# Kernel tuning notes

Hardware: AMD Instinct MI355X
Metric: run time of the kernel (lower is better)

Reference implementation:

```python
import jax, jax.numpy as jnp
import numpy as np

B, S, E, H = 2, 2048, 2048, 16
D = E // H          # head_dim = 128
RD = 128            # rotary_emb_dim (== head_dim here)
BASE = 10000.0


def setup_inputs() -> dict:
    key = jax.random.key(0)
    k1, k2, k3, k4, k5 = jax.random.split(key, 5)
    scale = 0.02
    return {
        "x": jax.random.normal(k1, (B, S, E), dtype=jnp.float32),
        "wqkv_w": jax.random.normal(k2, (3 * E, E), dtype=jnp.float32) * scale,
        "wqkv_b": jax.random.normal(k3, (3 * E,), dtype=jnp.float32) * scale,
        "out_w": jax.random.normal(k4, (E, E), dtype=jnp.float32) * scale,
        "out_b": jax.random.normal(k5, (E,), dtype=jnp.float32) * scale,
    }


def _rope_cos_sin(seqlen, dtype):
    inv_freq = 1.0 / (BASE ** (jnp.arange(0, RD, 2, dtype=jnp.float32) / RD))
    t = jnp.arange(seqlen, dtype=jnp.float32)
    freqs = jnp.outer(t, inv_freq)          # (S, RD//2)
    return jnp.cos(freqs).astype(dtype), jnp.sin(freqs).astype(dtype)


def _apply_rotary(v, cos, sin):
    # v: (B, S, H, D); rotate first RD dims (here RD == D)
    v_rot, v_pass = v[..., :RD], v[..., RD:]
    v1, v2 = jnp.split(v_rot, 2, axis=-1)    # each (B, S, H, RD//2)
    c = cos[None, :, None, :]
    s = sin[None, :, None, :]
    rot = jnp.concatenate([v1 * c - v2 * s, v1 * s + v2 * c], axis=-1)
    return jnp.concatenate([rot, v_pass], axis=-1)


def reference(x, wqkv_w, wqkv_b, out_w, out_b):
    b, s, e = x.shape
    # column-parallel QKV projection (world size 1)
    qkv = jnp.einsum("bse,fe->bsf", x, wqkv_w) + wqkv_b     # (B, S, 3E)
    qkv = qkv.reshape(b, s, 3, H, D)
    cos, sin = _rope_cos_sin(s, x.dtype)
    q = _apply_rotary(qkv[:, :, 0], cos, sin)               # (B, S, H, D)
    k = _apply_rotary(qkv[:, :, 1], cos, sin)
    v = qkv[:, :, 2]
    # causal self-attention, softmax_scale = 1/sqrt(head_dim)
    scale = 1.0 / jnp.sqrt(jnp.asarray(D, dtype=x.dtype))
    scores = jnp.einsum("bshd,bthd->bhst", q, k) * scale    # (B, H, S, S)
    causal_mask = jnp.tril(jnp.ones((s, s), dtype=bool))
    scores = jnp.where(causal_mask[None, None], scores, jnp.finfo(x.dtype).min)
    probs = jax.nn.softmax(scores, axis=-1)
    ctx = jnp.einsum("bhst,bthd->bshd", probs, v)           # (B, S, H, D)
    # row-parallel output projection
    out = jnp.einsum("bse,fe->bsf", ctx.reshape(b, s, e), out_w) + out_b
    return out
```

## Files before the change

### kernel.cpp

```cpp
#include <hip/hip_runtime.h>
#include <cstdint>
#include <cstddef>

#define Bd 2
#define Sd 2048
#define Ed 2048
#define Hd 16
#define Dd 128
#define N3E 6144
#define ATT_SCALE 0.08838834764831845f

typedef short bf16x8 __attribute__((ext_vector_type(8)));
typedef float f32x4 __attribute__((ext_vector_type(4)));

__device__ __forceinline__ float bf2f(unsigned short u) {
    union { unsigned int u; float f; } c;
    c.u = ((unsigned int)u) << 16;
    return c.f;
}
__device__ __forceinline__ unsigned short f2bf(float f) {
    union { float f; unsigned int u; } c;
    c.f = f;
    unsigned int x = c.u;
    x += 0x7FFFu + ((x >> 16) & 1u);
    return (unsigned short)(x >> 16);
}

__device__ __forceinline__ void gl2lds16(const void* g, void* l) {
    __builtin_amdgcn_global_load_lds(
        (const __attribute__((address_space(1))) void*)g,
        (__attribute__((address_space(3))) void*)l, 16, 0, 0);
}

__global__ void cvt_all(const float* __restrict__ x,
                        const float* __restrict__ w1,
                        const float* __restrict__ w2,
                        unsigned short* __restrict__ ox,
                        unsigned short* __restrict__ o1,
                        unsigned short* __restrict__ o2) {
    int i = (blockIdx.x * 256 + threadIdx.x) * 4;
    const float* s;
    unsigned short* d;
    int off;
    if (i < 8388608) { s = x; d = ox; off = i; }
    else if (i < 20971520) { s = w1; d = o1; off = i - 8388608; }
    else { s = w2; d = o2; off = i - 20971520; }
    const float4 v = *(const float4*)(s + off);
    d[off + 0] = f2bf(v.x);
    d[off + 1] = f2bf(v.y);
    d[off + 2] = f2bf(v.z);
    d[off + 3] = f2bf(v.w);
}

template <int MODE>
__global__ void gemm_bt(const unsigned short* __restrict__ A,
                        const unsigned short* __restrict__ Bm,
                        const float* __restrict__ bias,
                        void* __restrict__ o0, void* __restrict__ o1,
                        void* __restrict__ o2, int Ndim, int K) {
    __shared__ __align__(16) unsigned short U[16640];
    unsigned short* As = U;
    unsigned short* Bs = U + 8192;

    const int tid = threadIdx.x;
    const int lane = tid & 63;
    const int wave = tid >> 6;
    const int quad = lane >> 4;
    const int l16 = lane & 15;
    const int wr = wave >> 1;
    const int wc = wave & 1;

    const int n0 = blockIdx.x * 128;
    const int m0 = blockIdx.y * 128;

    const unsigned short* Ab = A + (size_t)m0 * K;
    const unsigned short* Bb = Bm + (size_t)n0 * K;

    const f32x4 fzero = {0.f, 0.f, 0.f, 0.f};
    f32x4 acc[4][4];
#pragma unroll
    for (int i = 0; i < 4; i++)
#pragma unroll
        for (int j = 0; j < 4; j++) acc[i][j] = fzero;

    for (int k0 = 0; k0 < K; k0 += 64) {
        __syncthreads();
#pragma unroll
        for (int it = 0; it < 4; ++it) {
            int L = it * 256 + tid;
            int row = L >> 3;
            int cs = L & 7;
            int gc = cs ^ (row & 7);
            gl2lds16(Ab + row * K + k0 + gc * 8, (void*)(As + L * 8));
            gl2lds16(Bb + row * K + k0 + gc * 8, (void*)(Bs + L * 8));
        }
        __syncthreads();
#pragma unroll
        for (int kk = 0; kk < 2; ++kk) {
            bf16x8 af[4], bfr[4];
#pragma unroll
            for (int i = 0; i < 4; i++) {
                int row = wr * 64 + i * 16 + l16;
                int cs = kk * 4 + quad;
                af[i] = *(const bf16x8*)(As + row * 64 + (cs ^ (row & 7)) * 8);
            }
#pragma unroll
            for (int j = 0; j < 4; j++) {
                int row = wc * 64 + j * 16 + l16;
                int cs = kk * 4 + quad;
                bfr[j] = *(const bf16x8*)(Bs + row * 64 + (cs ^ (row & 7)) * 8);
            }
#pragma unroll
            for (int i = 0; i < 4; i++)
#pragma unroll
                for (int j = 0; j < 4; j++)
                    acc[i][j] = __builtin_amdgcn_mfma_f32_16x16x32_bf16(
                        af[i], bfr[j], acc[i][j], 0, 0, 0);
        }
    }

    if (MODE == 0) {
#pragma unroll
        for (int j = 0; j < 4; j++) {
            int col = n0 + wc * 64 + j * 16 + l16;
            float bv = bias[col];
#pragma unroll
            for (int i = 0; i < 4; i++) {
                int rbase = m0 + wr * 64 + i * 16 + quad * 4;
#pragma unroll
                for (int r = 0; r < 4; r++)
                    ((float*)o0)[(size_t)(rbase + r) * Ndim + col] =
                        acc[i][j][r] + bv;
            }
        }
    } else {
        __syncthreads();
#pragma unroll
        for (int j = 0; j < 4; j++) {
            int coll = wc * 64 + j * 16 + l16;
            float bv = bias[n0 + coll];
#pragma unroll
            for (int i = 0; i < 4; i++) {
                int rl = wr * 64 + i * 16 + quad * 4;
#pragma unroll
                for (int r = 0; r < 4; r++)
                    U[(rl + r) * 130 + coll] = f2bf(acc[i][j][r] + bv);
            }
        }
        __syncthreads();

        const int ch = n0 >> 7;
        const int c = ch >> 4;
        const int h = ch & 15;
        const int bb = m0 >> 11;
        const int s0 = m0 & 2047;

        if (c < 2) {
            unsigned short* dstq = (unsigned short*)(c == 0 ? o0 : o1);
            const size_t hb = ((size_t)(bb * Hd + h)) * Sd;
#pragma unroll
            for (int it = 0; it < 16; ++it) {
                int lin = it * 256 + tid;
                int row = lin >> 5, p = lin & 31;
                int s = s0 + row;
                unsigned int lo = *(const unsigned int*)(U + row * 130 + 2 * p);
                unsigned int hi =
                    *(const unsigned int*)(U + row * 130 + 64 + 2 * p);
                float v1a = bf2f((unsigned short)lo), v1b = bf2f(lo >> 16);
                float v2a = bf2f((unsigned short)hi), v2b = bf2f(hi >> 16);
                float fa = (float)s * __expf(-(float)(2 * p) *
                                             (9.210340371976184f / 64.0f));
                float fb = (float)s * __expf(-(float)(2 * p + 1) *
                                             (9.210340371976184f / 64.0f));
                float sna, csa, snb, csb;
                __sincosf(fa, &sna, &csa);
                __sincosf(fb, &snb, &csb);
                ushort2 r1, r2;
                r1.x = f2bf(v1a * csa - v2a * sna);
                r1.y = f2bf(v1b * csb - v2b * snb);
                r2.x = f2bf(v1a * sna + v2a * csa);
                r2.y = f2bf(v1b * snb + v2b * csb);
                unsigned short* dst = dstq + (hb + s) * Dd;
                *(ushort2*)(dst + 2 * p) = r1;
                *(ushort2*)(dst + 64 + 2 * p) = r2;
            }
        } else {
            unsigned short* dstv = (unsigned short*)o2;
            const size_t hb = ((size_t)(bb * Hd + h)) * Dd;
#pragma unroll
            for (int it = 0; it < 16; ++it) {
                int lin = it * 256 + tid;
                int d = lin >> 5, sc = lin & 31;
                int s4 = sc * 4;
                ushort4 pk;
                pk.x = U[(s4 + 0) * 130 + d];
                pk.y = U[(s4 + 1) * 130 + d];
                pk.z = U[(s4 + 2) * 130 + d];
                pk.w = U[(s4 + 3) * 130 + d];
                *(ushort4*)(dstv + (hb + d) * Sd + s0 + s4) = pk;
            }
        }
    }
}

__global__ __launch_bounds__(256, 4) void flash_attn(
    const unsigned short* __restrict__ q, const unsigned short* __restrict__ k,
    const unsigned short* __restrict__ vt, unsigned short* __restrict__ ctx) {
    __shared__ __align__(16) unsigned short Ks[64 * 128];
    __shared__ __align__(16) unsigned short Vts[128 * 64];
    __shared__ __align__(16) unsigned short Ps[64 * 64];

    const int tid = threadIdx.x;
    const int lane = tid & 63;
    const int wave = tid >> 6;
    const int quad = lane >> 4;
    const int l16 = lane & 15;
    const int rw0 = wave * 16;
    const int ql = rw0 + l16;
    const int qsw = ql & 7;

    const int yy = blockIdx.y;
    const int kq = yy >> 3, y0 = yy & 7;
    const int qi = (kq == 0) ? 31 - y0 : (kq == 1) ? y0 : (kq == 2) ? 23 - y0 : 8 + y0;
    const int bh = blockIdx.x;
    const int q0 = qi * 64;

    const unsigned short* qb = q + ((size_t)bh * Sd + q0) * Dd;
    const unsigned short* kb = k + (size_t)bh * Sd * Dd;
    const unsigned short* vtb = vt + (size_t)bh * Dd * Sd;

#pragma unroll
    for (int it = 0; it < 4; ++it) {
        int L = it * 256 + tid;
        int row = L >> 4;
        int cs = L & 15;
        int gc = cs ^ (row & 15);
        gl2lds16(qb + row * Dd + gc * 8, (void*)(Ks + L * 8));
    }
    __syncthreads();
    bf16x8 aq[4];
#pragma unroll
    for (int kk = 0; kk < 4; kk++)
        aq[kk] = *(const bf16x8*)(Ks + ql * 128 + ((kk * 4 + quad) ^ (ql & 15)) * 8);
    __syncthreads();

    const f32x4 fzero = {0.f, 0.f, 0.f, 0.f};
    f32x4 o[8];
#pragma unroll
    for (int jd = 0; jd < 8; jd++) o[jd] = fzero;
    float mi = -3.0e38f, li = 0.f;

    for (int t0 = 0; t0 <= q0; t0 += 64) {
#pragma unroll
        for (int it = 0; it < 4; ++it) {
            int L = it * 256 + tid;
            int rk = L >> 4;
            int ck = L & 15;
            int gk = ck ^ (rk & 15);
            gl2lds16(kb + (size_t)(t0 + rk) * Dd + gk * 8, (void*)(Ks + L * 8));
            int rv = L >> 3;
            int cv = L & 7;
            int gv = cv ^ (rv & 7);
            gl2lds16(vtb + (size_t)rv * Sd + t0 + gv * 8, (void*)(Vts + L * 8));
        }
        __syncthreads();

        f32x4 sa[4];
#pragma unroll
        for (int j = 0; j < 4; j++) sa[j] = fzero;
#pragma unroll
        for (int kk = 0; kk < 4; kk++) {
            bf16x8 bk[4];
#pragma unroll
            for (int j = 0; j < 4; j++) {
                int rowt = j * 16 + l16;
                bk[j] = *(const bf16x8*)(Ks + rowt * 128 +
                                         ((kk * 4 + quad) ^ (rowt & 15)) * 8);
            }
#pragma unroll
            for (int j = 0; j < 4; j++)
                sa[j] = __builtin_amdgcn_mfma_f32_16x16x32_bf16(bk[j], aq[kk],
                                                                sa[j], 0, 0, 0);
        }

#pragma unroll
        for (int j = 0; j < 4; j++)
#pragma unroll
            for (int r = 0; r < 4; r++) sa[j][r] *= ATT_SCALE;
        if (t0 == q0) {
            const int qg = rw0 + l16;
#pragma unroll
            for (int j = 0; j < 4; j++)
#pragma unroll
                for (int r = 0; r < 4; r++)
                    if ((j * 16 + quad * 4 + r) > qg) sa[j][r] = -3.0e38f;
        }

        float mx = -3.0e38f;
#pragma unroll
        for (int j = 0; j < 4; j++)
#pragma unroll
            for (int r = 0; r < 4; r++) mx = fmaxf(mx, sa[j][r]);
        mx = fmaxf(mx, __shfl_xor(mx, 16, 64));
        mx = fmaxf(mx, __shfl_xor(mx, 32, 64));
        const float mnew = fmaxf(mi, mx);
        const float alpha = __expf(mi - mnew);
        float rs = 0.f;
#pragma unroll
        for (int j = 0; j < 4; j++)
#pragma unroll
            for (int r = 0; r < 4; r++) {
                float pp = __expf(sa[j][r] - mnew);
                sa[j][r] = pp;
                rs += pp;
            }
        rs += __shfl_xor(rs, 16, 64);
        rs += __shfl_xor(rs, 32, 64);
        li = li * alpha + rs;
        mi = mnew;

#pragma unroll
        for (int j = 0; j < 4; j++) {
            ushort4 pk;
            pk.x = f2bf(sa[j][0]);
            pk.y = f2bf(sa[j][1]);
            pk.z = f2bf(sa[j][2]);
            pk.w = f2bf(sa[j][3]);
            *(ushort4*)(Ps + ql * 64 + ((j * 2 + (quad >> 1)) ^ qsw) * 8 +
                        (quad & 1) * 4) = pk;
        }

        float av[4];
#pragma unroll
        for (int r = 0; r < 4; r++) av[r] = __shfl(alpha, quad * 4 + r, 64);
#pragma unroll
        for (int jd = 0; jd < 8; jd++)
#pragma unroll
            for (int r = 0; r < 4; r++) o[jd][r] *= av[r];

#pragma unroll
        for (int kk = 0; kk < 2; kk++) {
            bf16x8 ap = *(const bf16x8*)(Ps + ql * 64 +
                                         ((kk * 4 + quad) ^ qsw) * 8);
            bf16x8 bv[8];
#pragma unroll
            for (int jd = 0; jd < 8; jd++) {
                int d = jd * 16 + l16;
                bv[jd] = *(const bf16x8*)(Vts + d * 64 +
                                          ((kk * 4 + quad) ^ (d & 7)) * 8);
            }
#pragma unroll
            for (int jd = 0; jd < 8; jd++)
                o[jd] = __builtin_amdgcn_mfma_f32_16x16x32_bf16(ap, bv[jd],
                                                                o[jd], 0, 0, 0);
        }
        __syncthreads();
    }

    const int b = bh >> 4;
    const int h = bh & 15;
    float linv[4];
#pragma unroll
    for (int r = 0; r < 4; r++) linv[r] = 1.0f / __shfl(li, quad * 4 + r, 64);
#pragma unroll
    for (int r = 0; r < 4; r++) {
        const int grow = q0 + rw0 + quad * 4 + r;
        unsigned short* dst = ctx + ((size_t)(b * Sd + grow)) * Ed + h * Dd;
#pragma unroll
        for (int jd = 0; jd < 8; jd++)
            dst[jd * 16 + l16] = f2bf(o[jd][r] * linv[r]);
    }
}

extern "C" void kernel_launch(void* const* d_in, const int* in_sizes, int n_in,
                              void* d_out, int out_size, void* d_ws,
                              size_t ws_size, hipStream_t stream) {
    const float* x = (const float*)d_in[0];
    const float* wqkv_w = (const float*)d_in[1];
    const float* wqkv_b = (const float*)d_in[2];
    const float* out_w = (const float*)d_in[3];
    const float* out_b = (const float*)d_in[4];
    float* out = (float*)d_out;

    char* ws = (char*)d_ws;
    unsigned short* xb    = (unsigned short*)(ws + 0);
    unsigned short* wqkvb = (unsigned short*)(ws + 16777216);
    unsigned short* owb   = (unsigned short*)(ws + 41943040);
    unsigned short* qb    = (unsigned short*)(ws + 50331648);
    unsigned short* kb    = (unsigned short*)(ws + 67108864);
    unsigned short* vtb   = (unsigned short*)(ws + 83886080);
    unsigned short* ctx   = (unsigned short*)(ws + 0);

    cvt_all<<<24576, 256, 0, stream>>>(x, wqkv_w, out_w, xb, wqkvb, owb);
    gemm_bt<1><<<dim3(48, 32), 256, 0, stream>>>(xb, wqkvb, wqkv_b, qb, kb, vtb,
                                                 N3E, Ed);
    flash_attn<<<dim3(32, 32), 256, 0, stream>>>(qb, kb, vtb, ctx);
    gemm_bt<0><<<dim3(16, 32), 256, 0, stream>>>(ctx, owb, out_b, out, nullptr,
                                                 nullptr, Ed, Ed);
}
```

Before: 350.8 us.

## Use 128-row query tiles with 32x32 MFMA in flash attention

The flash attention kernel now processes 128 query rows per block (32 per wave) instead of 64, and switches from 16x16x32 to 32x32x16 bf16 MFMA for both QK^T and PV. Q is loaded straight from global memory into registers, masking is applied per element on every tile, and the grid halves to 16 query tiles per head. Larger tiles reuse each K/V tile across twice as many query rows, cutting LDS and global traffic per FLOP. The cost is higher register pressure (launch bounds lowered to 2), an extra barrier per iteration, wasted work on the diagonal tiles, and fewer blocks.

```diff
diff --git a/kernel.cpp b/kernel.cpp
--- a/kernel.cpp
+++ b/kernel.cpp
@@ -12,6 +12,7 @@
 
 typedef short bf16x8 __attribute__((ext_vector_type(8)));
 typedef float f32x4 __attribute__((ext_vector_type(4)));
+typedef float f32x16 __attribute__((ext_vector_type(16)));
 
 __device__ __forceinline__ float bf2f(unsigned short u) {
     union { unsigned int u; float f; } c;
@@ -203,54 +204,47 @@
     }
 }
 
-__global__ __launch_bounds__(256, 4) void flash_attn(
+__global__ __launch_bounds__(256, 2) void flash_attn(
     const unsigned short* __restrict__ q, const unsigned short* __restrict__ k,
     const unsigned short* __restrict__ vt, unsigned short* __restrict__ ctx) {
     __shared__ __align__(16) unsigned short Ks[64 * 128];
     __shared__ __align__(16) unsigned short Vts[128 * 64];
-    __shared__ __align__(16) unsigned short Ps[64 * 64];
+    __shared__ __align__(16) unsigned short Ps[128 * 64];
 
     const int tid = threadIdx.x;
     const int lane = tid & 63;
     const int wave = tid >> 6;
-    const int quad = lane >> 4;
-    const int l16 = lane & 15;
-    const int rw0 = wave * 16;
-    const int ql = rw0 + l16;
-    const int qsw = ql & 7;
+    const int l32 = lane & 31;
+    const int half = lane >> 5;
 
     const int yy = blockIdx.y;
-    const int kq = yy >> 3, y0 = yy & 7;
-    const int qi = (kq == 0) ? 31 - y0 : (kq == 1) ? y0 : (kq == 2) ? 23 - y0 : 8 + y0;
+    const int qi = (yy < 8) ? 15 - yy : yy - 8;
     const int bh = blockIdx.x;
-    const int q0 = qi * 64;
-
-    const unsigned short* qb = q + ((size_t)bh * Sd + q0) * Dd;
+    const int q0 = qi * 128;
+    const int qg = q0 + wave * 32 + l32;
+    const int prow = wave * 32 + l32;
+    const int psw = prow & 7;
+
     const unsigned short* kb = k + (size_t)bh * Sd * Dd;
     const unsigned short* vtb = vt + (size_t)bh * Dd * Sd;
 
-#pragma unroll
-    for (int it = 0; it < 4; ++it) {
-        int L = it * 256 + tid;
-        int row = L >> 4;
-        int cs = L & 15;
-        int gc = cs ^ (row & 15);
-        gl2lds16(qb + row * Dd + gc * 8, (void*)(Ks + L * 8));
+    bf16x8 aq[8];
+    {
+        const unsigned short* qrow = q + ((size_t)bh * Sd + qg) * Dd;
+#pragma unroll
+        for (int ks = 0; ks < 8; ks++)
+            aq[ks] = *(const bf16x8*)(qrow + ks * 16 + half * 8);
     }
-    __syncthreads();
-    bf16x8 aq[4];
-#pragma unroll
-    for (int kk = 0; kk < 4; kk++)
-        aq[kk] = *(const bf16x8*)(Ks + ql * 128 + ((kk * 4 + quad) ^ (ql & 15)) * 8);
-    __syncthreads();
-
-    const f32x4 fzero = {0.f, 0.f, 0.f, 0.f};
-    f32x4 o[8];
-#pragma unroll
-    for (int jd = 0; jd < 8; jd++) o[jd] = fzero;
+
+    f32x16 o[4];
+#pragma unroll
+    for (int db = 0; db < 4; db++)
+#pragma unroll
+        for (int r = 0; r < 16; r++) o[db][r] = 0.f;
     float mi = -3.0e38f, li = 0.f;
 
-    for (int t0 = 0; t0 <= q0; t0 += 64) {
+    const int tmax = q0 + 64;
+    for (int t0 = 0; t0 <= tmax; t0 += 64) {
 #pragma unroll
         for (int it = 0; it < 4; ++it) {
             int L = it * 256 + tid;
@@ -265,111 +259,101 @@
         }
         __syncthreads();
 
-        f32x4 sa[4];
-#pragma unroll
-        for (int j = 0; j < 4; j++) sa[j] = fzero;
-#pragma unroll
-        for (int kk = 0; kk < 4; kk++) {
-            bf16x8 bk[4];
-#pragma unroll
-            for (int j = 0; j < 4; j++) {
-                int rowt = j * 16 + l16;
-                bk[j] = *(const bf16x8*)(Ks + rowt * 128 +
-                                         ((kk * 4 + quad) ^ (rowt & 15)) * 8);
-            }
-#pragma unroll
-            for (int j = 0; j < 4; j++)
-                sa[j] = __builtin_amdgcn_mfma_f32_16x16x32_bf16(bk[j], aq[kk],
-                                                                sa[j], 0, 0, 0);
-        }
-
-#pragma unroll
-        for (int j = 0; j < 4; j++)
-#pragma unroll
-            for (int r = 0; r < 4; r++) sa[j][r] *= ATT_SCALE;
-        if (t0 == q0) {
-            const int qg = rw0 + l16;
-#pragma unroll
-            for (int j = 0; j < 4; j++)
-#pragma unroll
-                for (int r = 0; r < 4; r++)
-                    if ((j * 16 + quad * 4 + r) > qg) sa[j][r] = -3.0e38f;
+        f32x16 sa[2];
+#pragma unroll
+        for (int b2 = 0; b2 < 2; b2++)
+#pragma unroll
+            for (int r = 0; r < 16; r++) sa[b2][r] = 0.f;
+#pragma unroll
+        for (int ks = 0; ks < 8; ks++) {
+            int cd = ks * 2 + half;
+#pragma unroll
+            for (int b2 = 0; b2 < 2; b2++) {
+                int row = b2 * 32 + l32;
+                bf16x8 ak = *(const bf16x8*)(Ks + row * 128 +
+                                             (cd ^ (row & 15)) * 8);
+                sa[b2] = __builtin_amdgcn_mfma_f32_32x32x16_bf16(ak, aq[ks],
+                                                                 sa[b2], 0, 0, 0);
+            }
         }
 
         float mx = -3.0e38f;
 #pragma unroll
-        for (int j = 0; j < 4; j++)
-#pragma unroll
-            for (int r = 0; r < 4; r++) mx = fmaxf(mx, sa[j][r]);
-        mx = fmaxf(mx, __shfl_xor(mx, 16, 64));
+        for (int b2 = 0; b2 < 2; b2++)
+#pragma unroll
+            for (int r = 0; r < 16; r++) {
+                float v = sa[b2][r] * ATT_SCALE;
+                int tg = t0 + b2 * 32 + (r & 3) + 8 * (r >> 2) + 4 * half;
+                if (tg > qg) v = -3.0e38f;
+                sa[b2][r] = v;
+                mx = fmaxf(mx, v);
+            }
         mx = fmaxf(mx, __shfl_xor(mx, 32, 64));
         const float mnew = fmaxf(mi, mx);
         const float alpha = __expf(mi - mnew);
         float rs = 0.f;
 #pragma unroll
-        for (int j = 0; j < 4; j++)
-#pragma unroll
-            for (int r = 0; r < 4; r++) {
-                float pp = __expf(sa[j][r] - mnew);
-                sa[j][r] = pp;
+        for (int b2 = 0; b2 < 2; b2++)
+#pragma unroll
+            for (int r = 0; r < 16; r++) {
+                float pp = __expf(sa[b2][r] - mnew);
+                sa[b2][r] = pp;
                 rs += pp;
             }
-        rs += __shfl_xor(rs, 16, 64);
         rs += __shfl_xor(rs, 32, 64);
         li = li * alpha + rs;
         mi = mnew;
 
 #pragma unroll
-        for (int j = 0; j < 4; j++) {
-            ushort4 pk;
-            pk.x = f2bf(sa[j][0]);
-            pk.y = f2bf(sa[j][1]);
-            pk.z = f2bf(sa[j][2]);
-            pk.w = f2bf(sa[j][3]);
-            *(ushort4*)(Ps + ql * 64 + ((j * 2 + (quad >> 1)) ^ qsw) * 8 +
-                        (quad & 1) * 4) = pk;
-        }
-
-        float av[4];
-#pragma unroll
-        for (int r = 0; r < 4; r++) av[r] = __shfl(alpha, quad * 4 + r, 64);
-#pragma unroll
-        for (int jd = 0; jd < 8; jd++)
-#pragma unroll
-            for (int r = 0; r < 4; r++) o[jd][r] *= av[r];
-
-#pragma unroll
-        for (int kk = 0; kk < 2; kk++) {
-            bf16x8 ap = *(const bf16x8*)(Ps + ql * 64 +
-                                         ((kk * 4 + quad) ^ qsw) * 8);
-            bf16x8 bv[8];
-#pragma unroll
-            for (int jd = 0; jd < 8; jd++) {
-                int d = jd * 16 + l16;
-                bv[jd] = *(const bf16x8*)(Vts + d * 64 +
-                                          ((kk * 4 + quad) ^ (d & 7)) * 8);
-            }
-#pragma unroll
-            for (int jd = 0; jd < 8; jd++)
-                o[jd] = __builtin_amdgcn_mfma_f32_16x16x32_bf16(ap, bv[jd],
-                                                                o[jd], 0, 0, 0);
+        for (int db = 0; db < 4; db++)
+#pragma unroll
+            for (int r = 0; r < 16; r++) o[db][r] *= alpha;
+
+#pragma unroll
+        for (int b2 = 0; b2 < 2; b2++)
+#pragma unroll
+            for (int g = 0; g < 4; g++) {
+                ushort4 pk;
+                pk.x = f2bf(sa[b2][g * 4 + 0]);
+                pk.y = f2bf(sa[b2][g * 4 + 1]);
+                pk.z = f2bf(sa[b2][g * 4 + 2]);
+                pk.w = f2bf(sa[b2][g * 4 + 3]);
+                *(ushort4*)(Ps + prow * 64 + ((b2 * 4 + g) ^ psw) * 8 +
+                            half * 4) = pk;
+            }
+        __syncthreads();
+
+#pragma unroll
+        for (int kk = 0; kk < 4; kk++) {
+            bf16x8 bp = *(const bf16x8*)(Ps + prow * 64 +
+                                         ((kk * 2 + half) ^ psw) * 8);
+#pragma unroll
+            for (int db = 0; db < 4; db++) {
+                int row = db * 32 + l32;
+                bf16x8 av = *(const bf16x8*)(
+                    Vts + row * 64 + ((kk * 2 + half) ^ (row & 7)) * 8);
+                o[db] = __builtin_amdgcn_mfma_f32_32x32x16_bf16(av, bp, o[db],
+                                                                0, 0, 0);
+            }
         }
         __syncthreads();
     }
 
     const int b = bh >> 4;
     const int h = bh & 15;
-    float linv[4];
-#pragma unroll
-    for (int r = 0; r < 4; r++) linv[r] = 1.0f / __shfl(li, quad * 4 + r, 64);
-#pragma unroll
-    for (int r = 0; r < 4; r++) {
-        const int grow = q0 + rw0 + quad * 4 + r;
-        unsigned short* dst = ctx + ((size_t)(b * Sd + grow)) * Ed + h * Dd;
-#pragma unroll
-        for (int jd = 0; jd < 8; jd++)
-            dst[jd * 16 + l16] = f2bf(o[jd][r] * linv[r]);
-    }
+    const float inv = 1.0f / li;
+    unsigned short* dst = ctx + ((size_t)(b * Sd + qg)) * Ed + h * Dd;
+#pragma unroll
+    for (int db = 0; db < 4; db++)
+#pragma unroll
+        for (int g = 0; g < 4; g++) {
+            ushort4 pk;
+            pk.x = f2bf(o[db][g * 4 + 0] * inv);
+            pk.y = f2bf(o[db][g * 4 + 1] * inv);
+            pk.z = f2bf(o[db][g * 4 + 2] * inv);
+            pk.w = f2bf(o[db][g * 4 + 3] * inv);
+            *(ushort4*)(dst + db * 32 + g * 8 + half * 4) = pk;
+        }
 }
 
 extern "C" void kernel_launch(void* const* d_in, const int* in_sizes, int n_in,
@@ -394,7 +378,7 @@
     cvt_all<<<24576, 256, 0, stream>>>(x, wqkv_w, out_w, xb, wqkvb, owb);
     gemm_bt<1><<<dim3(48, 32), 256, 0, stream>>>(xb, wqkvb, wqkv_b, qb, kb, vtb,
                                                  N3E, Ed);
-    flash_attn<<<dim3(32, 32), 256, 0, stream>>>(qb, kb, vtb, ctx);
+    flash_attn<<<dim3(32, 16), 256, 0, stream>>>(qb, kb, vtb, ctx);
     gemm_bt<0><<<dim3(16, 32), 256, 0, stream>>>(ctx, owb, out_b, out, nullptr,
                                                  nullptr, Ed, Ed);
 }
```

Result: no change. 348.5 us (-0.7%).
